# Kernel optimization log

Measured on AMD Instinct MI355X. Metric: run time of the kernel, lower is better.

The kernel has to match this reference:

```python
import jax, jax.numpy as jnp
import numpy as np

B, C, H, W = 4, 256, 64, 64


def _radius_bias(h, w):
    # Attention_Radius: grid coords (x: 1..W, y: H..1), pairwise euclidean dist
    y = jnp.arange(h, 0, -1, dtype=jnp.float32)
    x = jnp.arange(1, w + 1, dtype=jnp.float32)
    yy, xx = jnp.meshgrid(y, x, indexing='ij')
    coords = jnp.stack([xx.reshape(-1), yy.reshape(-1)], axis=1)  # [N,2]
    diff = coords[:, None, :] - coords[None, :, :]                # [N,N,2]
    dist = jnp.sqrt(jnp.sum(diff * diff, axis=-1))                # [N,N]
    # Weight_Mapping: linearly map to [0.5,2] with inversion (far -> small)
    lo, hi = jnp.float32(0.5), jnp.float32(2.0)
    return hi - (dist - dist.min()) * (hi - lo) / (dist.max() - dist.min())


def setup_inputs() -> dict:
    key = jax.random.key(0)
    k1, k2, k3, k4 = jax.random.split(key, 4)
    scale = 1.0 / np.sqrt(C)
    return {
        'x': jax.random.normal(k1, (B, C, H, W), dtype=jnp.float32),
        'w_phi': jax.random.normal(k2, (C, C), dtype=jnp.float32) * scale,
        'w_theta': jax.random.normal(k3, (C, C), dtype=jnp.float32) * scale,
        'w_g': jax.random.normal(k4, (C, C), dtype=jnp.float32) * scale,
    }


def reference(x, w_phi, w_theta, w_g):
    b, c, h, w = x.shape
    n = h * w
    xf = x.reshape(b, c, n)                                  # [b,c,N]
    phi = jnp.einsum('dc,bcn->bdn', w_phi, xf)               # [b,c,N]
    theta = jnp.einsum('dc,bcn->bnd', w_theta, xf)           # [b,N,c]
    g = jnp.einsum('dc,bcn->bnd', w_g, xf)                   # [b,N,c]
    scores = jnp.einsum('bnc,bcm->bnm', theta, phi)          # [b,N,N]
    scores = _radius_bias(h, w) * scores                     # multiplicative radius bias
    attn = jax.nn.softmax(scores, axis=1)                    # NOTE: softmax over dim=1 (rows)
    out = jnp.einsum('bnm,bmc->bnc', attn, g)                # [b,N,c]
    out = out.transpose(0, 2, 1).reshape(b, c, h, w)
    return out + x
```

## Files before the change

kernel.cpp:

```cpp
#include <hip/hip_runtime.h>
#include <math.h>

typedef unsigned short ush;
typedef short short8 __attribute__((ext_vector_type(8)));
typedef int i32x4 __attribute__((ext_vector_type(4)));
typedef int i32x16 __attribute__((ext_vector_type(16)));
typedef float f32x16 __attribute__((ext_vector_type(16)));
typedef unsigned int u32;

namespace {
constexpr int B = 4, C = 256, N = 4096, NCH = 4;
constexpr size_t PL8 = (size_t)B * N * C;
constexpr size_t OFF_TH  = 0;
constexpr size_t OFF_TL  = PL8;
constexpr size_t OFF_PH  = 2 * PL8;
constexpr size_t OFF_PLO = 3 * PL8;
constexpr size_t OFF_G   = 4 * PL8;
constexpr size_t FOFF    = 4 * PL8 + (size_t)B * C * N * 2;
constexpr size_t F_PM = 0;
constexpr size_t F_PS = (size_t)B * NCH * N;
constexpr size_t F_M  = 2 * (size_t)B * NCH * N;

constexpr size_t OFF_XH = 26ull * 1024 * 1024;
constexpr size_t OFF_XL = OFF_XH + (size_t)B * N * C * 2;
constexpr size_t OFF_WH = OFF_XL + (size_t)B * N * C * 2;
constexpr size_t OFF_WL = OFF_WH + (size_t)3 * C * C * 2;
constexpr size_t WS_NEED = OFF_WL + (size_t)3 * C * C * 2;

constexpr float SCL = 8.0f / 127.0f;
constexpr float S2  = SCL * SCL;
constexpr float RB  = 1.5f / 89.09545f;
constexpr float L2E = 1.44269504f;
constexpr float BA2  = 2.0f * S2 * L2E;
constexpr float BBC2 = RB * S2 * L2E;
constexpr float C1  = 1.0f / 254.0f;
constexpr float INV_SCL = 127.0f / 8.0f;
}

#define MFMAI8(a, b, c)  __builtin_amdgcn_mfma_i32_32x32x32_i8((a), (b), (c), 0, 0, 0)
#define MFMABF(a, b, c)  __builtin_amdgcn_mfma_f32_32x32x16_bf16((a), (b), (c), 0, 0, 0)

#define WAITV(n) asm volatile("s_waitcnt vmcnt(" #n ")" ::: "memory")
#define WAITVL(n) asm volatile("s_waitcnt vmcnt(" #n ") lgkmcnt(0)" ::: "memory")
#define PBAR __builtin_amdgcn_s_barrier()

__device__ __forceinline__ float fast_exp2(float x) {
#if __has_builtin(__builtin_amdgcn_exp2f)
  return __builtin_amdgcn_exp2f(x);
#else
  float r; asm("v_exp_f32 %0, %1" : "=v"(r) : "v"(x)); return r;
#endif
}
__device__ __forceinline__ float fast_sqrt(float x) {
#if __has_builtin(__builtin_amdgcn_sqrtf)
  return __builtin_amdgcn_sqrtf(x);
#else
  float r; asm("v_sqrt_f32 %0, %1" : "=v"(r) : "v"(x)); return r;
#endif
}

__device__ __forceinline__ ush f2bf(float v) {
  u32 x = __float_as_uint(v);
  return (ush)((x + 0x7FFFu + ((x >> 16) & 1u)) >> 16);
}
__device__ __forceinline__ float bf2f(ush h) {
  return __uint_as_float(((u32)h) << 16);
}

__device__ __forceinline__ float score_i(int hh, int xx, int d2i) {
  float u = fmaf((float)xx, C1, (float)hh);
  float d = fast_sqrt((float)d2i);
  return fmaf(d, -BBC2, BA2) * u;
}

__device__ __forceinline__ void gload16(const void* g, void* l) {
  __builtin_amdgcn_global_load_lds(
      (const __attribute__((address_space(1))) u32*)(g),
      (__attribute__((address_space(3))) u32*)(l), 16, 0, 0);
}


__global__ __launch_bounds__(256) void proj_kernel(
    const float* __restrict__ x, const float* __restrict__ w_phi,
    const float* __restrict__ w_theta, const float* __restrict__ w_g,
    char* __restrict__ wsu8) {
  __shared__ float Wst[16][68];
  __shared__ float Xs[16][68];
  const int tid = threadIdx.x, tx = tid & 15, ty = tid >> 4;
  const int b = blockIdx.y / 3, p = blockIdx.y % 3;
  const int c0 = (blockIdx.x >> 6) * 64;
  const int nb = (blockIdx.x & 63) * 64;
  const float* w = (p == 0) ? w_theta : (p == 1) ? w_phi : w_g;

  float acc[4][4] = {};
  for (int kk = 0; kk < C; kk += 16) {
    {
      int r = tid >> 2, kq = (tid & 3) << 2;
      float4 v = *reinterpret_cast<const float4*>(&w[(size_t)(c0 + r) * C + kk + kq]);
      Wst[kq + 0][r] = v.x; Wst[kq + 1][r] = v.y;
      Wst[kq + 2][r] = v.z; Wst[kq + 3][r] = v.w;
    }
    {
      int k = tid >> 4, j4 = (tid & 15) << 2;
      *reinterpret_cast<float4*>(&Xs[k][j4]) =
          *reinterpret_cast<const float4*>(&x[((size_t)b * C + kk + k) * N + nb + j4]);
    }
    __syncthreads();
#pragma unroll
    for (int k2 = 0; k2 < 16; ++k2) {
      float4 av = *reinterpret_cast<const float4*>(&Wst[k2][ty << 2]);
      float4 bv = *reinterpret_cast<const float4*>(&Xs[k2][tx << 2]);
      float aa[4] = {av.x, av.y, av.z, av.w};
      float bb[4] = {bv.x, bv.y, bv.z, bv.w};
#pragma unroll
      for (int i = 0; i < 4; ++i)
#pragma unroll
        for (int j = 0; j < 4; ++j) acc[i][j] = fmaf(aa[i], bb[j], acc[i][j]);
    }
    __syncthreads();
  }

  if (p < 2) {
    char* hi = wsu8 + (p == 0 ? OFF_TH : OFF_PH) + (size_t)b * N * C;
    char* lo = wsu8 + (p == 0 ? OFF_TL : OFF_PLO) + (size_t)b * N * C;
    const int k0 = c0 + (ty << 2);
    const size_t koff = (size_t)(k0 >> 5) * 1024 + ((k0 >> 4) & 1) * 512 + (k0 & 15);
#pragma unroll
    for (int j = 0; j < 4; ++j) {
      int n = nb + (tx << 2) + j;
      u32 ph = 0, pl = 0;
#pragma unroll
      for (int i = 0; i < 4; ++i) {
        float t = acc[i][j] * INV_SCL;
        int h = __float2int_rn(t);
        h = max(-127, min(127, h));
        int l = __float2int_rn((t - (float)h) * 254.0f);
        l = max(-127, min(127, l));
        ph |= ((u32)(h & 0xFF)) << (8 * i);
        pl |= ((u32)(l & 0xFF)) << (8 * i);
      }
      size_t a = (size_t)(n >> 5) * 8192 + (size_t)(n & 31) * 16 + koff;
      *(u32*)(hi + a) = ph;
      *(u32*)(lo + a) = pl;
    }
  } else {
    ush* gp = (ush*)(wsu8 + OFF_G) + (size_t)b * C * N;
#pragma unroll
    for (int i = 0; i < 4; ++i) {
      ushort4 pk;
      pk.x = f2bf(acc[i][0]); pk.y = f2bf(acc[i][1]);
      pk.z = f2bf(acc[i][2]); pk.w = f2bf(acc[i][3]);
      *reinterpret_cast<ushort4*>(&gp[(size_t)(c0 + (ty << 2) + i) * N + nb + (tx << 2)]) = pk;
    }
  }
}

__global__ __launch_bounds__(256) void split_x(
    const float* __restrict__ x, char* __restrict__ wsu8) {
  __shared__ float Ls[64 * 66];
  const int tid = threadIdx.x;
  const int n0 = blockIdx.x * 64, c0 = blockIdx.y * 64, b = blockIdx.z;
  const float* xb = x + ((size_t)b * C + c0) * N + n0;
#pragma unroll
  for (int i = 0; i < 4; ++i) {
    int fi = i * 256 + tid, cc = fi >> 4, c4 = fi & 15;
    float4 v = *reinterpret_cast<const float4*>(xb + (size_t)cc * N + c4 * 4);
    Ls[cc * 66 + c4 * 4 + 0] = v.x; Ls[cc * 66 + c4 * 4 + 1] = v.y;
    Ls[cc * 66 + c4 * 4 + 2] = v.z; Ls[cc * 66 + c4 * 4 + 3] = v.w;
  }
  __syncthreads();
  ush* XH = (ush*)(wsu8 + OFF_XH) + ((size_t)b * N + n0) * C + c0;
  ush* XL = (ush*)(wsu8 + OFF_XL) + ((size_t)b * N + n0) * C + c0;
#pragma unroll
  for (int i = 0; i < 4; ++i) {
    int oi = i * 256 + tid, n = oi >> 4, c4 = oi & 15;
    ushort4 hv, lv;
#pragma unroll
    for (int j = 0; j < 4; ++j) {
      float v = Ls[(c4 * 4 + j) * 66 + n];
      ush h = f2bf(v);
      ush l = f2bf(v - bf2f(h));
      (&hv.x)[j] = h; (&lv.x)[j] = l;
    }
    *reinterpret_cast<ushort4*>(XH + (size_t)n * C + c4 * 4) = hv;
    *reinterpret_cast<ushort4*>(XL + (size_t)n * C + c4 * 4) = lv;
  }
}

__global__ __launch_bounds__(256) void split_w(
    const float* __restrict__ w_phi, const float* __restrict__ w_theta,
    const float* __restrict__ w_g, char* __restrict__ wsu8) {
  int id = blockIdx.x * 256 + threadIdx.x;
  int p = id / 16384, e4 = id % 16384;
  const float* w = (p == 0) ? w_theta : (p == 1) ? w_phi : w_g;
  float4 v = *reinterpret_cast<const float4*>(w + (size_t)e4 * 4);
  ush* WH = (ush*)(wsu8 + OFF_WH) + (size_t)p * C * C + (size_t)e4 * 4;
  ush* WL = (ush*)(wsu8 + OFF_WL) + (size_t)p * C * C + (size_t)e4 * 4;
  ushort4 hv, lv;
  float vv[4] = {v.x, v.y, v.z, v.w};
#pragma unroll
  for (int j = 0; j < 4; ++j) {
    ush h = f2bf(vv[j]);
    ush l = f2bf(vv[j] - bf2f(h));
    (&hv.x)[j] = h; (&lv.x)[j] = l;
  }
  *reinterpret_cast<ushort4*>(WH) = hv;
  *reinterpret_cast<ushort4*>(WL) = lv;
}

__global__ __launch_bounds__(512) void proj_mfma(char* __restrict__ wsu8) {
  __shared__ __align__(16) char plds[131072];
  const int tid = threadIdx.x, lane = tid & 63, w = tid >> 6;
  const int l31 = lane & 31, lh5 = lane >> 5;
  const int wr = w >> 2, wc = w & 3;
  const int bx = blockIdx.x;
  const int db = (bx >> 5) * 64, nb = (bx & 31) * 128;
  const int b = blockIdx.y / 3, p = blockIdx.y % 3;
  const char* xh = wsu8 + OFF_XH + (size_t)b * N * C * 2;
  const char* xl = wsu8 + OFF_XL + (size_t)b * N * C * 2;
  const char* wh = wsu8 + OFF_WH + (size_t)p * C * C * 2;
  const char* wl = wsu8 + OFF_WL + (size_t)p * C * C * 2;
  char* const Wb = plds;
  char* const Xb = plds + 65536;

#pragma unroll
  for (int cix = 0; cix < 8; ++cix) {
    int pl = cix >> 2, ci = cix & 3;
    int glin = ci * 512 + tid;
    int d = glin >> 5, g = glin & 31;
    const char* src = (pl ? wl : wh) + (size_t)(db + d) * 512 + ((g ^ (d & 15)) << 4);
    gload16(src, Wb + pl * 32768 + ci * 8192 + (tid << 4));
  }
  auto stageX = [&](int ch, int buf) {
#pragma unroll
    for (int cix = 0; cix < 4; ++cix) {
      int pl = cix >> 1, ci = cix & 1;
      int glin = ci * 512 + tid;
      int n = glin >> 3, g = glin & 7;
      const char* src = (pl ? xl : xh) +
          (size_t)(nb + n) * 512 + ch * 128 + ((g ^ (n & 7)) << 4);
      gload16(src, Xb + buf * 32768 + pl * 16384 + ci * 8192 + (tid << 4));
    }
  };
  stageX(0, 0);
  __syncthreads();

  const int arow = wr * 32 + l31;
  const int brow = wc * 32 + l31;
  f32x16 acc = {};
  for (int ch = 0; ch < 4; ++ch) {
    if (ch < 3) stageX(ch + 1, (ch + 1) & 1);
    const char* XB = Xb + (ch & 1) * 32768;
    __builtin_amdgcn_s_setprio(1);
#pragma unroll
    for (int kt = 0; kt < 4; ++kt) {
      int slw = (ch * 4 + kt) * 2 + lh5;
      int oW = ((slw ^ (arow & 15)) << 4);
      short8 wa = *(const short8*)(Wb + arow * 512 + oW);
      short8 wb2 = *(const short8*)(Wb + 32768 + arow * 512 + oW);
      int slx = kt * 2 + lh5;
      int oX = ((slx ^ (brow & 7)) << 4);
      short8 xa = *(const short8*)(XB + brow * 128 + oX);
      short8 xb2 = *(const short8*)(XB + 16384 + brow * 128 + oX);
      acc = MFMABF(wa, xa, acc);
      acc = MFMABF(wa, xb2, acc);
      acc = MFMABF(wb2, xa, acc);
    }
    __builtin_amdgcn_s_setprio(0);
    __syncthreads();
  }

  const int n = nb + wc * 32 + l31;
  if (p < 2) {
    char* hi = wsu8 + (p == 0 ? OFF_TH : OFF_PH) + (size_t)b * N * C;
    char* lo = wsu8 + (p == 0 ? OFF_TL : OFF_PLO) + (size_t)b * N * C;
#pragma unroll
    for (int q = 0; q < 4; ++q) {
      u32 phv = 0, plv = 0;
#pragma unroll
      for (int j = 0; j < 4; ++j) {
        float t = acc[q * 4 + j] * INV_SCL;
        int h = __float2int_rn(t);
        h = max(-127, min(127, h));
        int l = __float2int_rn((t - (float)h) * 254.0f);
        l = max(-127, min(127, l));
        phv |= ((u32)(h & 0xFF)) << (8 * j);
        plv |= ((u32)(l & 0xFF)) << (8 * j);
      }
      int dd = db + wr * 32 + 8 * q + 4 * lh5;
      size_t a = (size_t)(n >> 5) * 8192 + (size_t)(dd >> 5) * 1024 +
                 ((dd >> 4) & 1) * 512 + (size_t)(n & 31) * 16 + (dd & 15);
      *(u32*)(hi + a) = phv;
      *(u32*)(lo + a) = plv;
    }
  } else {
    ush* gp = (ush*)(wsu8 + OFF_G) + (size_t)b * C * N;
#pragma unroll
    for (int r = 0; r < 16; ++r) {
      int dd = db + wr * 32 + (r & 3) + 8 * (r >> 2) + 4 * lh5;
      gp[(size_t)dd * N + n] = f2bf(acc[r]);
    }
  }
}

__global__ __launch_bounds__(512, 4) void stats_kernel(
    const char* __restrict__ wsu8, float* __restrict__ fws) {
  __shared__ __align__(16) char lds[65536];
  const int tid = threadIdx.x, lane = tid & 63, w = tid >> 6;
  const int l31 = lane & 31, lh5 = lane >> 5;
  const int wr = w >> 2, wc = w & 3;
  int flat = (blockIdx.z * NCH + blockIdx.y) * 32 + blockIdx.x;
  int nf = ((flat & 7) << 6) | (flat >> 3);
  const int b = nf >> 7, rem = nf & 127, chunk = rem >> 5, mt = rem & 31;
  const int mb = mt * 128, cbase = chunk * 1024;
  const size_t bo = (size_t)b * N * C;
  const char* th  = wsu8 + OFF_TH + bo;
  const char* tl  = wsu8 + OFF_TL + bo;
  const char* ph  = wsu8 + OFF_PH + bo;
  const char* plo = wsu8 + OFF_PLO + bo;

  const int brow = wc * 32 + l31;
  i32x4 FH[8];
  {
    const char* prh = ph + (size_t)((mb >> 5) + wc) * 8192 + lh5 * 512 + l31 * 16;
#pragma unroll
    for (int q = 0; q < 8; ++q) FH[q] = *(const i32x4*)(prh + q * 1024);
  }
#pragma unroll
  for (int i = 0; i < 4; ++i)
    gload16(plo + (size_t)(mb >> 5) * 8192 + i * 8192 + tid * 16,
            lds + i * 8192 + tid * 16);
  char* const T0 = lds + 32768;
  char* const T1 = lds + 49152;

  auto stage = [&](int s, char* dst) {
    int ntx = s >> 1, h = s & 1;
    int g2 = tid >> 8;
    int inr = (tid & 255) * 16;
#pragma unroll
    for (int plane = 0; plane < 2; ++plane) {
      const char* src = (plane ? tl : th) +
          (size_t)((cbase >> 5) + ntx * 2 + g2) * 8192 + h * 4096 + inr;
      gload16(src, dst + plane * 8192 + g2 * 4096 + inr);
    }
  };
  stage(0, T0);
  __syncthreads();

  const int m = mb + brow;
  const int mcl = m & 63, mh = m >> 6;
  const int nbl = wr * 32;
  float rmax = -3e38f, rsum = 0.0f;

  u32 dxp[8];
#pragma unroll
  for (int r2 = 0; r2 < 8; ++r2) {
    int r0i = 2 * r2, r1i = 2 * r2 + 1;
    int p0 = (r0i & 3) + 8 * (r0i >> 2) + 4 * lh5;
    int p1 = (r1i & 3) + 8 * (r1i >> 2) + 4 * lh5;
    int d0 = nbl + p0 - mcl, d1 = nbl + p1 - mcl;
    dxp[r2] = (u32)(d0 * d0) | ((u32)(d1 * d1) << 16);
  }

  char* Tc = T0; char* Tn = T1;
  for (int nt = 0; nt < 16; ++nt) {
    i32x16 HH = {}, XX = {};
#pragma unroll
    for (int h = 0; h < 2; ++h) {
      int p = nt * 2 + h;
      if (p < 31) stage(p + 1, Tn);
      __builtin_amdgcn_s_setprio(1);
#pragma unroll
      for (int kt = 0; kt < 4; ++kt) {
        int g = h * 4 + kt;
        const char* aB = Tc + wr * 4096 + kt * 1024 + lh5 * 512 + l31 * 16;
        i32x4 ah = *(const i32x4*)(aB);
        i32x4 al = *(const i32x4*)(aB + 8192);
        i32x4 bl = *(const i32x4*)(lds + wc * 8192 + g * 1024 + lh5 * 512 + l31 * 16);
        HH = MFMAI8(ah, FH[g], HH);
        XX = MFMAI8(ah, bl, XX);
        XX = MFMAI8(al, FH[g], XX);
      }
      __builtin_amdgcn_s_setprio(0);
      if (h == 1) {
        int dyi = (cbase >> 6) + nt - mh;
        int dy2i = dyi * dyi;
        float bs[16];
#pragma unroll
        for (int r = 0; r < 16; ++r) {
          int d2i = (int)((dxp[r >> 1] >> ((r & 1) * 16)) & 0xFFFFu) + dy2i;
          bs[r] = score_i(HH[r], XX[r], d2i);
        }
        float m0 = fmaxf(fmaxf(fmaxf(bs[0], bs[1]), fmaxf(bs[2], bs[3])),
                         fmaxf(fmaxf(bs[4], bs[5]), fmaxf(bs[6], bs[7])));
        float m1 = fmaxf(fmaxf(fmaxf(bs[8], bs[9]), fmaxf(bs[10], bs[11])),
                         fmaxf(fmaxf(bs[12], bs[13]), fmaxf(bs[14], bs[15])));
        float nm = fmaxf(rmax, fmaxf(m0, m1));
#pragma unroll
        for (int r = 0; r < 16; ++r) bs[r] = fast_exp2(bs[r] - nm);
        float s0 = ((bs[0] + bs[1]) + (bs[2] + bs[3])) + ((bs[4] + bs[5]) + (bs[6] + bs[7]));
        float s1 = ((bs[8] + bs[9]) + (bs[10] + bs[11])) + ((bs[12] + bs[13]) + (bs[14] + bs[15]));
        rsum = fmaf(rsum, fast_exp2(rmax - nm), s0 + s1);
        rmax = nm;
      }
      __syncthreads();
      char* t = Tc; Tc = Tn; Tn = t;
    }
  }
  {
    float om = __shfl_xor(rmax, 32);
    float os = __shfl_xor(rsum, 32);
    float nm = fmaxf(rmax, om);
    rsum = rsum * fast_exp2(rmax - nm) + os * fast_exp2(om - nm);
    rmax = nm;
  }
  float* redM = (float*)lds;
  float* redS = (float*)(lds + 1024);
  if (lane < 32) {
    redM[wr * 128 + wc * 32 + l31] = rmax;
    redS[wr * 128 + wc * 32 + l31] = rsum;
  }
  __syncthreads();
  if (tid < 128) {
    float m0 = redM[tid], m1 = redM[128 + tid];
    float nm = fmaxf(m0, m1);
    float s = redS[tid] * fast_exp2(m0 - nm) + redS[128 + tid] * fast_exp2(m1 - nm);
    fws[F_PM + ((size_t)(b * NCH + chunk)) * N + mb + tid] = nm;
    fws[F_PS + ((size_t)(b * NCH + chunk)) * N + mb + tid] = s;
  }
}

__global__ __launch_bounds__(256) void finalize_stats(float* __restrict__ fws) {
  int id = blockIdx.x * 256 + threadIdx.x;
  if (id >= B * N) return;
  int b = id >> 12, m = id & (N - 1);
  float M = -3e38f;
#pragma unroll
  for (int ch = 0; ch < NCH; ++ch)
    M = fmaxf(M, fws[F_PM + (size_t)(b * NCH + ch) * N + m]);
  float S = 0.0f;
#pragma unroll
  for (int ch = 0; ch < NCH; ++ch)
    S += fws[F_PS + (size_t)(b * NCH + ch) * N + m] *
         fast_exp2(fws[F_PM + (size_t)(b * NCH + ch) * N + m] - M);
  fws[F_M + id] = M + __log2f(S);
}

__global__ __launch_bounds__(512, 1) void out_kernel(
    const float* __restrict__ x, float* __restrict__ out,
    const char* __restrict__ wsu8, const float* __restrict__ fws) {
  __shared__ __align__(16) char lds[98304];
  const int tid = threadIdx.x, lane = tid & 63, w = tid >> 6;
  const int l31 = lane & 31, lh5 = lane >> 5;
  const int wn = w >> 2, wm = w & 3;
  int flat = blockIdx.y * gridDim.x + blockIdx.x;
  int nf = ((flat & 7) << 5) | (flat >> 3);
  const int b = nf >> 6, ntile = nf & 63;
  const int n0 = ntile * 64;
  const size_t bo = (size_t)b * N * C;
  const char* th  = wsu8 + OFF_TH + bo;
  const char* tl  = wsu8 + OFF_TL + bo;
  const char* ph  = wsu8 + OFF_PH + bo;
  const char* plo = wsu8 + OFF_PLO + bo;
  const char* GPB = wsu8 + OFF_G + (size_t)b * C * N * 2;
  const float* Qv = fws + F_M + (size_t)b * N;

  char* const Ga = lds;
  char* const Gb = lds + 32768;
  char* const Pb = lds + 65536;
  char* const Qb = lds + 81920;

  const int grow = w * 32 + l31;
  const int gswz = grow & 7;
  const int pcol = wm * 32 + l31;
  const int mcl = pcol & 63;

  i32x4 TH[8], TL[8];
  {
    const char* trh = th + (size_t)((n0 >> 5) + wn) * 8192 + lh5 * 512 + l31 * 16;
    const char* trl = tl + (size_t)((n0 >> 5) + wn) * 8192 + lh5 * 512 + l31 * 16;
#pragma unroll
    for (int q = 0; q < 8; ++q) {
      TH[q] = *(const i32x4*)(trh + q * 1024);
      TL[q] = *(const i32x4*)(trl + q * 1024);
    }
  }
  u32 dxp[8];
#pragma unroll
  for (int r2 = 0; r2 < 8; ++r2) {
    int r0i = 2 * r2, r1i = 2 * r2 + 1;
    int p0i = wn * 32 + (r0i & 3) + 8 * (r0i >> 2) + 4 * lh5;
    int p1i = wn * 32 + (r1i & 3) + 8 * (r1i >> 2) + 4 * lh5;
    int d0 = p0i - mcl, d1 = p1i - mcl;
    dxp[r2] = (u32)(d0 * d0) | ((u32)(d1 * d1) << 16);
  }
#pragma unroll
  for (int i = 0; i < 2; ++i)
    gload16((const char*)Qv + i * 8192 + w * 1024 + lane * 16,
            Qb + i * 8192 + w * 1024 + lane * 16);

  i32x4 Bh[8], Bl[8];
  auto ldphi = [&](int m0i) {
    const char* sph = ph  + (size_t)((m0i >> 5) + wm) * 8192 + lh5 * 512 + l31 * 16;
    const char* spl = plo + (size_t)((m0i >> 5) + wm) * 8192 + lh5 * 512 + l31 * 16;
#pragma unroll
    for (int q = 0; q < 8; ++q) {
      Bh[q] = *(const i32x4*)(sph + q * 1024);
      Bl[q] = *(const i32x4*)(spl + q * 1024);
    }
  };
  auto stageG = [&](int m0g, char* dst) {
#pragma unroll
    for (int cix = 0; cix < 4; ++cix) {
      int rl = cix * 64 + w * 8 + (lane >> 3);
      int gc = lane & 7;
      const char* src = GPB + (size_t)rl * (N * 2) + (size_t)m0g * 2 + ((gc ^ (rl & 7)) << 4);
      gload16(src, dst + cix * 8192 + w * 1024 + lane * 16);
    }
  };

  ldphi(0);
  WAITV(0);
  PBAR;

  f32x16 oacc0 = {}, oacc1 = {};

  for (int mc = 0; mc < 32; ++mc) {
    const int m0 = mc * 128;
    const int mg = m0 + pcol;
    const float Qm = *(const float*)(Qb + 4 * mg);
    i32x16 HH = {}, XX = {};

    stageG(m0, Ga);
    __builtin_amdgcn_s_setprio(1);
#pragma unroll
    for (int kt = 0; kt < 4; ++kt) {
      HH = MFMAI8(TH[kt], Bh[kt], HH);
      XX = MFMAI8(TH[kt], Bl[kt], XX);
      XX = MFMAI8(TL[kt], Bh[kt], XX);
    }
    __builtin_amdgcn_s_setprio(0);
    stageG(m0 + 64, Gb);
    __builtin_amdgcn_s_setprio(1);
#pragma unroll
    for (int kt = 4; kt < 8; ++kt) {
      HH = MFMAI8(TH[kt], Bh[kt], HH);
      XX = MFMAI8(TH[kt], Bl[kt], XX);
      XX = MFMAI8(TL[kt], Bh[kt], XX);
    }
    __builtin_amdgcn_s_setprio(0);
    {
      const int gP = pcol >> 3, bP = (pcol & 7) << 1;
      int dyi = ntile - (mg >> 6);
      int dy2i = dyi * dyi;
#pragma unroll
      for (int r = 0; r < 16; ++r) {
        int prow = wn * 32 + (r & 3) + 8 * (r >> 2) + 4 * lh5;
        int d2i = (int)((dxp[r >> 1] >> ((r & 1) * 16)) & 0xFFFFu) + dy2i;
        float bs = score_i(HH[r], XX[r], d2i);
        float pv = fast_exp2(bs - Qm);
        *(ush*)(Pb + prow * 256 + (((gP ^ (prow & 15)) << 4)) + bP) = f2bf(pv);
      }
    }
    WAITVL(4); PBAR;

    if (mc < 31) ldphi(m0 + 128);
    __builtin_amdgcn_s_setprio(1);
#pragma unroll
    for (int t2 = 0; t2 < 4; ++t2) {
      int gG = (((t2 * 2 + lh5) ^ gswz) << 4);
      short8 gb = *(const short8*)(Ga + grow * 128 + gG);
      {
        int gP0 = ((((t2 * 2 + lh5) ^ (l31 & 15)) << 4));
        short8 pa = *(const short8*)(Pb + l31 * 256 + gP0);
        oacc0 = MFMABF(pa, gb, oacc0);
      }
      {
        int ar = 32 + l31;
        int gP1 = ((((t2 * 2 + lh5) ^ (ar & 15)) << 4));
        short8 pa = *(const short8*)(Pb + ar * 256 + gP1);
        oacc1 = MFMABF(pa, gb, oacc1);
      }
    }
    __builtin_amdgcn_s_setprio(0);
    if (mc < 31) { WAITV(16); } else { WAITV(0); }
    PBAR;

    __builtin_amdgcn_s_setprio(1);
#pragma unroll
    for (int t2 = 0; t2 < 4; ++t2) {
      int gG = (((t2 * 2 + lh5) ^ gswz) << 4);
      short8 gb = *(const short8*)(Gb + grow * 128 + gG);
      {
        int gP0 = ((((8 + t2 * 2 + lh5) ^ (l31 & 15)) << 4));
        short8 pa = *(const short8*)(Pb + l31 * 256 + gP0);
        oacc0 = MFMABF(pa, gb, oacc0);
      }
      {
        int ar = 32 + l31;
        int gP1 = ((((8 + t2 * 2 + lh5) ^ (ar & 15)) << 4));
        short8 pa = *(const short8*)(Pb + ar * 256 + gP1);
        oacc1 = MFMABF(pa, gb, oacc1);
      }
    }
    __builtin_amdgcn_s_setprio(0);
    PBAR;
  }

  float* Tr = (float*)lds;
  const int c = w * 32 + l31;
#pragma unroll
  for (int r = 0; r < 16; ++r) {
    int crow = (r & 3) + 8 * (r >> 2) + 4 * lh5;
    Tr[c * 65 + crow] = oacc0[r];
    Tr[c * 65 + 32 + crow] = oacc1[r];
  }
  __syncthreads();
  const float* xb = x + (size_t)b * C * N;
  float* ob = out + (size_t)b * C * N;
  for (int e = tid; e < 16384; e += 512) {
    int cc = e >> 6, nl = e & 63;
    size_t idx = (size_t)cc * N + n0 + nl;
    ob[idx] = Tr[cc * 65 + nl] + xb[idx];
  }
}

extern "C" void kernel_launch(void* const* d_in, const int* in_sizes, int n_in,
                              void* d_out, int out_size, void* d_ws, size_t ws_size,
                              hipStream_t stream) {
  const float* x       = (const float*)d_in[0];
  const float* w_phi   = (const float*)d_in[1];
  const float* w_theta = (const float*)d_in[2];
  const float* w_g     = (const float*)d_in[3];
  float* out = (float*)d_out;
  char* wsu8 = (char*)d_ws;
  float* fws = (float*)(wsu8 + FOFF);

  if (ws_size >= WS_NEED) {
    split_x<<<dim3(64, 4, 4), 256, 0, stream>>>(x, wsu8);
    split_w<<<dim3(192), 256, 0, stream>>>(w_phi, w_theta, w_g, wsu8);
    proj_mfma<<<dim3(128, 12), 512, 0, stream>>>(wsu8);
  } else {
    proj_kernel<<<dim3(256, 12), 256, 0, stream>>>(x, w_phi, w_theta, w_g, wsu8);
  }
  stats_kernel<<<dim3(32, NCH, B), 512, 0, stream>>>(wsu8, fws);
  finalize_stats<<<dim3(B * N / 256), 256, 0, stream>>>(fws);
  out_kernel<<<dim3(64, B), 512, 0, stream>>>(x, out, wsu8, fws);
}
```

Before: 220.8 us.

## Stage phi tiles through LDS with triple-buffered rotating regions

```diff
diff --git a/kernel.cpp b/kernel.cpp
--- a/kernel.cpp
+++ b/kernel.cpp
@@ -449,7 +449,7 @@
 __global__ __launch_bounds__(512, 1) void out_kernel(
     const float* __restrict__ x, float* __restrict__ out,
     const char* __restrict__ wsu8, const float* __restrict__ fws) {
-  __shared__ __align__(16) char lds[98304];
+  __shared__ __align__(16) char lds[131072];
   const int tid = threadIdx.x, lane = tid & 63, w = tid >> 6;
   const int l31 = lane & 31, lh5 = lane >> 5;
   const int wn = w >> 2, wm = w & 3;
@@ -465,10 +465,11 @@
   const char* GPB = wsu8 + OFF_G + (size_t)b * C * N * 2;
   const float* Qv = fws + F_M + (size_t)b * N;
 
-  char* const Ga = lds;
-  char* const Gb = lds + 32768;
-  char* const Pb = lds + 65536;
-  char* const Qb = lds + 81920;
+  char* const R0 = lds;
+  char* const R1 = lds + 32768;
+  char* const R2 = lds + 65536;
+  char* const Pb = lds + 98304;
+  char* const Qb = lds + 114688;
 
   const int grow = w * 32 + l31;
   const int gswz = grow & 7;
@@ -499,14 +500,15 @@
     gload16((const char*)Qv + i * 8192 + w * 1024 + lane * 16,
             Qb + i * 8192 + w * 1024 + lane * 16);
 
-  i32x4 Bh[8], Bl[8];
-  auto ldphi = [&](int m0i) {
-    const char* sph = ph  + (size_t)((m0i >> 5) + wm) * 8192 + lh5 * 512 + l31 * 16;
-    const char* spl = plo + (size_t)((m0i >> 5) + wm) * 8192 + lh5 * 512 + l31 * 16;
-#pragma unroll
-    for (int q = 0; q < 8; ++q) {
-      Bh[q] = *(const i32x4*)(sph + q * 1024);
-      Bl[q] = *(const i32x4*)(spl + q * 1024);
+  auto stagePhi = [&](int m0p, int h, char* dst) {
+#pragma unroll
+    for (int cix = 0; cix < 4; ++cix) {
+      int p2 = cix >> 1, mpair = cix & 1;
+      int mb2 = mpair * 2 + (tid >> 8);
+      int inr = (tid & 255) * 16;
+      const char* base = p2 ? plo : ph;
+      const char* src = base + (size_t)((m0p >> 5) + mb2) * 8192 + h * 4096 + inr;
+      gload16(src, dst + p2 * 16384 + mb2 * 4096 + inr);
     }
   };
   auto stageG = [&](int m0g, char* dst) {
@@ -519,34 +521,44 @@
     }
   };
 
-  ldphi(0);
-  WAITV(0);
+  stagePhi(0, 0, R0);
+  stagePhi(0, 1, R1);
+  WAITV(4);
   PBAR;
 
   f32x16 oacc0 = {}, oacc1 = {};
+  char* Bc = R0; char* Bn = R1; char* Bn2 = R2;
 
   for (int mc = 0; mc < 32; ++mc) {
     const int m0 = mc * 128;
+    i32x16 HH = {}, XX = {};
     const int mg = m0 + pcol;
     const float Qm = *(const float*)(Qb + 4 * mg);
-    i32x16 HH = {}, XX = {};
-
-    stageG(m0, Ga);
+
+    stageG(m0, Bn2);
     __builtin_amdgcn_s_setprio(1);
 #pragma unroll
     for (int kt = 0; kt < 4; ++kt) {
-      HH = MFMAI8(TH[kt], Bh[kt], HH);
-      XX = MFMAI8(TH[kt], Bl[kt], XX);
-      XX = MFMAI8(TL[kt], Bh[kt], XX);
+      const char* bB = Bc + wm * 4096 + kt * 1024 + lh5 * 512 + l31 * 16;
+      i32x4 bh = *(const i32x4*)(bB);
+      i32x4 bl = *(const i32x4*)(bB + 16384);
+      HH = MFMAI8(TH[kt], bh, HH);
+      XX = MFMAI8(TH[kt], bl, XX);
+      XX = MFMAI8(TL[kt], bh, XX);
     }
     __builtin_amdgcn_s_setprio(0);
-    stageG(m0 + 64, Gb);
+    WAITV(4); PBAR;
+
+    stageG(m0 + 64, Bc);
     __builtin_amdgcn_s_setprio(1);
 #pragma unroll
-    for (int kt = 4; kt < 8; ++kt) {
-      HH = MFMAI8(TH[kt], Bh[kt], HH);
-      XX = MFMAI8(TH[kt], Bl[kt], XX);
-      XX = MFMAI8(TL[kt], Bh[kt], XX);
+    for (int kt = 0; kt < 4; ++kt) {
+      const char* bB = Bn + wm * 4096 + kt * 1024 + lh5 * 512 + l31 * 16;
+      i32x4 bh = *(const i32x4*)(bB);
+      i32x4 bl = *(const i32x4*)(bB + 16384);
+      HH = MFMAI8(TH[4 + kt], bh, HH);
+      XX = MFMAI8(TH[4 + kt], bl, XX);
+      XX = MFMAI8(TL[4 + kt], bh, XX);
     }
     __builtin_amdgcn_s_setprio(0);
     {
@@ -564,12 +576,12 @@
     }
     WAITVL(4); PBAR;
 
-    if (mc < 31) ldphi(m0 + 128);
+    if (mc < 31) stagePhi(m0 + 128, 0, Bn);
     __builtin_amdgcn_s_setprio(1);
 #pragma unroll
     for (int t2 = 0; t2 < 4; ++t2) {
       int gG = (((t2 * 2 + lh5) ^ gswz) << 4);
-      short8 gb = *(const short8*)(Ga + grow * 128 + gG);
+      short8 gb = *(const short8*)(Bn2 + grow * 128 + gG);
       {
         int gP0 = ((((t2 * 2 + lh5) ^ (l31 & 15)) << 4));
         short8 pa = *(const short8*)(Pb + l31 * 256 + gP0);
@@ -583,14 +595,15 @@
       }
     }
     __builtin_amdgcn_s_setprio(0);
-    if (mc < 31) { WAITV(16); } else { WAITV(0); }
+    if (mc < 31) { WAITV(4); } else { WAITV(0); }
     PBAR;
 
+    if (mc < 31) stagePhi(m0 + 128, 1, Bn2);
     __builtin_amdgcn_s_setprio(1);
 #pragma unroll
     for (int t2 = 0; t2 < 4; ++t2) {
       int gG = (((t2 * 2 + lh5) ^ gswz) << 4);
-      short8 gb = *(const short8*)(Gb + grow * 128 + gG);
+      short8 gb = *(const short8*)(Bc + grow * 128 + gG);
       {
         int gP0 = ((((8 + t2 * 2 + lh5) ^ (l31 & 15)) << 4));
         short8 pa = *(const short8*)(Pb + l31 * 256 + gP0);
@@ -604,7 +617,10 @@
       }
     }
     __builtin_amdgcn_s_setprio(0);
+    if (mc < 31) { WAITV(4); } else { WAITV(0); }
     PBAR;
+
+    char* t = Bc; Bc = Bn; Bn = Bn2; Bn2 = t;
   }
 
   float* Tr = (float*)lds;
```

Measured after the change: 201.3 us (median of 2 runs). 8.8% less time.

## Restructure out_kernel into 32-row tiles with 4 waves and per-wave LDS staging

Applied to the files above, without the earlier changes.

```diff
diff --git a/kernel.cpp b/kernel.cpp
--- a/kernel.cpp
+++ b/kernel.cpp
@@ -41,7 +41,7 @@
 #define MFMABF(a, b, c)  __builtin_amdgcn_mfma_f32_32x32x16_bf16((a), (b), (c), 0, 0, 0)
 
 #define WAITV(n) asm volatile("s_waitcnt vmcnt(" #n ")" ::: "memory")
-#define WAITVL(n) asm volatile("s_waitcnt vmcnt(" #n ") lgkmcnt(0)" ::: "memory")
+#define WAITL0   asm volatile("s_waitcnt lgkmcnt(0)" ::: "memory")
 #define PBAR __builtin_amdgcn_s_barrier()
 
 __device__ __forceinline__ float fast_exp2(float x) {
@@ -446,17 +446,16 @@
   fws[F_M + id] = M + __log2f(S);
 }
 
-__global__ __launch_bounds__(512, 1) void out_kernel(
+__global__ __launch_bounds__(256, 2) void out_kernel(
     const float* __restrict__ x, float* __restrict__ out,
     const char* __restrict__ wsu8, const float* __restrict__ fws) {
-  __shared__ __align__(16) char lds[98304];
+  __shared__ __align__(16) char lds[73728];
   const int tid = threadIdx.x, lane = tid & 63, w = tid >> 6;
   const int l31 = lane & 31, lh5 = lane >> 5;
-  const int wn = w >> 2, wm = w & 3;
   int flat = blockIdx.y * gridDim.x + blockIdx.x;
-  int nf = ((flat & 7) << 5) | (flat >> 3);
-  const int b = nf >> 6, ntile = nf & 63;
-  const int n0 = ntile * 64;
+  int nf = ((flat & 7) << 6) | (flat >> 3);
+  const int b = nf >> 7, ntile = nf & 127;
+  const int n0 = ntile * 32;
   const size_t bo = (size_t)b * N * C;
   const char* th  = wsu8 + OFF_TH + bo;
   const char* tl  = wsu8 + OFF_TL + bo;
@@ -465,20 +464,17 @@
   const char* GPB = wsu8 + OFF_G + (size_t)b * C * N * 2;
   const float* Qv = fws + F_M + (size_t)b * N;
 
-  char* const Ga = lds;
-  char* const Gb = lds + 32768;
+  char* const WR = lds + w * 16384;
   char* const Pb = lds + 65536;
-  char* const Qb = lds + 81920;
-
-  const int grow = w * 32 + l31;
-  const int gswz = grow & 7;
-  const int pcol = wm * 32 + l31;
+
+  const int pcol = w * 32 + l31;
   const int mcl = pcol & 63;
+  const int nbl = (ntile & 1) * 32;
 
   i32x4 TH[8], TL[8];
   {
-    const char* trh = th + (size_t)((n0 >> 5) + wn) * 8192 + lh5 * 512 + l31 * 16;
-    const char* trl = tl + (size_t)((n0 >> 5) + wn) * 8192 + lh5 * 512 + l31 * 16;
+    const char* trh = th + (size_t)(n0 >> 5) * 8192 + lh5 * 512 + l31 * 16;
+    const char* trl = tl + (size_t)(n0 >> 5) * 8192 + lh5 * 512 + l31 * 16;
 #pragma unroll
     for (int q = 0; q < 8; ++q) {
       TH[q] = *(const i32x4*)(trh + q * 1024);
@@ -489,139 +485,102 @@
 #pragma unroll
   for (int r2 = 0; r2 < 8; ++r2) {
     int r0i = 2 * r2, r1i = 2 * r2 + 1;
-    int p0i = wn * 32 + (r0i & 3) + 8 * (r0i >> 2) + 4 * lh5;
-    int p1i = wn * 32 + (r1i & 3) + 8 * (r1i >> 2) + 4 * lh5;
-    int d0 = p0i - mcl, d1 = p1i - mcl;
+    int p0i = (r0i & 3) + 8 * (r0i >> 2) + 4 * lh5;
+    int p1i = (r1i & 3) + 8 * (r1i >> 2) + 4 * lh5;
+    int d0 = nbl + p0i - mcl, d1 = nbl + p1i - mcl;
     dxp[r2] = (u32)(d0 * d0) | ((u32)(d1 * d1) << 16);
   }
-#pragma unroll
-  for (int i = 0; i < 2; ++i)
-    gload16((const char*)Qv + i * 8192 + w * 1024 + lane * 16,
-            Qb + i * 8192 + w * 1024 + lane * 16);
-
-  i32x4 Bh[8], Bl[8];
-  auto ldphi = [&](int m0i) {
-    const char* sph = ph  + (size_t)((m0i >> 5) + wm) * 8192 + lh5 * 512 + l31 * 16;
-    const char* spl = plo + (size_t)((m0i >> 5) + wm) * 8192 + lh5 * 512 + l31 * 16;
+
+  auto stagePhiW = [&](int m0p) {
+    const char* s0 = ph  + (size_t)((m0p >> 5) + w) * 8192;
+    const char* s1 = plo + (size_t)((m0p >> 5) + w) * 8192;
+#pragma unroll
+    for (int i = 0; i < 8; ++i) {
+      gload16(s0 + i * 1024 + lane * 16, WR + i * 1024 + lane * 16);
+      gload16(s1 + i * 1024 + lane * 16, WR + 8192 + i * 1024 + lane * 16);
+    }
+  };
+  auto stageGW = [&](int m0g) {
+#pragma unroll
+    for (int s = 0; s < 2; ++s)
+#pragma unroll
+      for (int j = 0; j < 8; ++j) {
+        int cr = s * 128 + w * 32 + j * 4 + (lane >> 4);
+        int g = lane & 15;
+        const char* src = GPB + (size_t)cr * (N * 2) + (size_t)m0g * 2 +
+                          ((g ^ (cr & 15)) << 4);
+        gload16(src, WR + s * 8192 + j * 1024 + lane * 16);
+      }
+  };
+
+  stagePhiW(0);
+  f32x16 oacc0 = {}, oacc1 = {};
+
+  for (int mc = 0; mc < 32; ++mc) {
+    const int mg = mc * 128 + pcol;
+    const float Qm = Qv[mg];
+    i32x16 HH = {}, XX = {};
+    WAITV(0);
+    __builtin_amdgcn_s_setprio(1);
 #pragma unroll
     for (int q = 0; q < 8; ++q) {
-      Bh[q] = *(const i32x4*)(sph + q * 1024);
-      Bl[q] = *(const i32x4*)(spl + q * 1024);
-    }
-  };
-  auto stageG = [&](int m0g, char* dst) {
-#pragma unroll
-    for (int cix = 0; cix < 4; ++cix) {
-      int rl = cix * 64 + w * 8 + (lane >> 3);
-      int gc = lane & 7;
-      const char* src = GPB + (size_t)rl * (N * 2) + (size_t)m0g * 2 + ((gc ^ (rl & 7)) << 4);
-      gload16(src, dst + cix * 8192 + w * 1024 + lane * 16);
-    }
-  };
-
-  ldphi(0);
-  WAITV(0);
-  PBAR;
-
-  f32x16 oacc0 = {}, oacc1 = {};
-
-  for (int mc = 0; mc < 32; ++mc) {
-    const int m0 = mc * 128;
-    const int mg = m0 + pcol;
-    const float Qm = *(const float*)(Qb + 4 * mg);
-    i32x16 HH = {}, XX = {};
-
-    stageG(m0, Ga);
-    __builtin_amdgcn_s_setprio(1);
-#pragma unroll
-    for (int kt = 0; kt < 4; ++kt) {
-      HH = MFMAI8(TH[kt], Bh[kt], HH);
-      XX = MFMAI8(TH[kt], Bl[kt], XX);
-      XX = MFMAI8(TL[kt], Bh[kt], XX);
+      i32x4 bh = *(const i32x4*)(WR + q * 1024 + lh5 * 512 + l31 * 16);
+      i32x4 bl = *(const i32x4*)(WR + 8192 + q * 1024 + lh5 * 512 + l31 * 16);
+      HH = MFMAI8(TH[q], bh, HH);
+      XX = MFMAI8(TH[q], bl, XX);
+      XX = MFMAI8(TL[q], bh, XX);
     }
     __builtin_amdgcn_s_setprio(0);
-    stageG(m0 + 64, Gb);
-    __builtin_amdgcn_s_setprio(1);
-#pragma unroll
-    for (int kt = 4; kt < 8; ++kt) {
-      HH = MFMAI8(TH[kt], Bh[kt], HH);
-      XX = MFMAI8(TH[kt], Bl[kt], XX);
-      XX = MFMAI8(TL[kt], Bh[kt], XX);
-    }
-    __builtin_amdgcn_s_setprio(0);
+    WAITL0;
+    stageGW(mc * 128);
     {
       const int gP = pcol >> 3, bP = (pcol & 7) << 1;
-      int dyi = ntile - (mg >> 6);
+      int dyi = (ntile >> 1) - (mg >> 6);
       int dy2i = dyi * dyi;
 #pragma unroll
       for (int r = 0; r < 16; ++r) {
-        int prow = wn * 32 + (r & 3) + 8 * (r >> 2) + 4 * lh5;
+        int prow = (r & 3) + 8 * (r >> 2) + 4 * lh5;
         int d2i = (int)((dxp[r >> 1] >> ((r & 1) * 16)) & 0xFFFFu) + dy2i;
         float bs = score_i(HH[r], XX[r], d2i);
         float pv = fast_exp2(bs - Qm);
         *(ush*)(Pb + prow * 256 + (((gP ^ (prow & 15)) << 4)) + bP) = f2bf(pv);
       }
     }
-    WAITVL(4); PBAR;
-
-    if (mc < 31) ldphi(m0 + 128);
+    __syncthreads();
     __builtin_amdgcn_s_setprio(1);
 #pragma unroll
-    for (int t2 = 0; t2 < 4; ++t2) {
-      int gG = (((t2 * 2 + lh5) ^ gswz) << 4);
-      short8 gb = *(const short8*)(Ga + grow * 128 + gG);
+    for (int q = 0; q < 8; ++q) {
+      int mch = q * 2 + lh5;
+      short8 pa = *(const short8*)(Pb + l31 * 256 + ((mch ^ (l31 & 15)) << 4));
       {
-        int gP0 = ((((t2 * 2 + lh5) ^ (l31 & 15)) << 4));
-        short8 pa = *(const short8*)(Pb + l31 * 256 + gP0);
+        short8 gb = *(const short8*)(WR + l31 * 256 + ((mch ^ (l31 & 15)) << 4));
         oacc0 = MFMABF(pa, gb, oacc0);
       }
       {
-        int ar = 32 + l31;
-        int gP1 = ((((t2 * 2 + lh5) ^ (ar & 15)) << 4));
-        short8 pa = *(const short8*)(Pb + ar * 256 + gP1);
+        short8 gb = *(const short8*)(WR + 8192 + l31 * 256 + ((mch ^ (l31 & 15)) << 4));
         oacc1 = MFMABF(pa, gb, oacc1);
       }
     }
     __builtin_amdgcn_s_setprio(0);
-    if (mc < 31) { WAITV(16); } else { WAITV(0); }
-    PBAR;
-
-    __builtin_amdgcn_s_setprio(1);
-#pragma unroll
-    for (int t2 = 0; t2 < 4; ++t2) {
-      int gG = (((t2 * 2 + lh5) ^ gswz) << 4);
-      short8 gb = *(const short8*)(Gb + grow * 128 + gG);
-      {
-        int gP0 = ((((8 + t2 * 2 + lh5) ^ (l31 & 15)) << 4));
-        short8 pa = *(const short8*)(Pb + l31 * 256 + gP0);
-        oacc0 = MFMABF(pa, gb, oacc0);
-      }
-      {
-        int ar = 32 + l31;
-        int gP1 = ((((8 + t2 * 2 + lh5) ^ (ar & 15)) << 4));
-        short8 pa = *(const short8*)(Pb + ar * 256 + gP1);
-        oacc1 = MFMABF(pa, gb, oacc1);
-      }
-    }
-    __builtin_amdgcn_s_setprio(0);
-    PBAR;
+    __syncthreads();
+    if (mc < 31) stagePhiW((mc + 1) * 128);
   }
 
   float* Tr = (float*)lds;
-  const int c = w * 32 + l31;
+  const int cb = w * 32 + l31;
 #pragma unroll
   for (int r = 0; r < 16; ++r) {
-    int crow = (r & 3) + 8 * (r >> 2) + 4 * lh5;
-    Tr[c * 65 + crow] = oacc0[r];
-    Tr[c * 65 + 32 + crow] = oacc1[r];
+    int nr = (r & 3) + 8 * (r >> 2) + 4 * lh5;
+    Tr[cb * 33 + nr] = oacc0[r];
+    Tr[(128 + cb) * 33 + nr] = oacc1[r];
   }
   __syncthreads();
   const float* xb = x + (size_t)b * C * N;
   float* ob = out + (size_t)b * C * N;
-  for (int e = tid; e < 16384; e += 512) {
-    int cc = e >> 6, nl = e & 63;
+  for (int e = tid; e < 8192; e += 256) {
+    int cc = e >> 5, nl = e & 31;
     size_t idx = (size_t)cc * N + n0 + nl;
-    ob[idx] = Tr[cc * 65 + nl] + xb[idx];
+    ob[idx] = Tr[cc * 33 + nl] + xb[idx];
   }
 }
 
@@ -645,5 +604,5 @@
   }
   stats_kernel<<<dim3(32, NCH, B), 512, 0, stream>>>(wsu8, fws);
   finalize_stats<<<dim3(B * N / 256), 256, 0, stream>>>(fws);
-  out_kernel<<<dim3(64, B), 512, 0, stream>>>(x, out, wsu8, fws);
-}
+  out_kernel<<<dim3(128, B), 256, 0, stream>>>(x, out, wsu8, fws);
+}
```

After: 227.8 us. 1.03x slower.
